# Kernel tuning notes

Hardware: AMD Instinct MI355X
Metric: run time of the kernel (lower is better)

The kernel has to match this reference:

```python
import jax, jax.numpy as jnp
import numpy as np

EPS = 1e-5

def _conv(x, w, pad):
    return jax.lax.conv_general_dilated(
        x, w, window_strides=(1, 1), padding=[(pad, pad), (pad, pad)],
        dimension_numbers=('NCHW', 'OIHW', 'NCHW'))

def _bn(x, g, b):
    # training-mode batch norm over (N, H, W), matching nn.BatchNorm2d in train mode
    m = x.mean(axis=(0, 2, 3), keepdims=True)
    v = x.var(axis=(0, 2, 3), keepdims=True)
    return (x - m) * jax.lax.rsqrt(v + EPS) * g[None, :, None, None] + b[None, :, None, None]

def setup_inputs() -> dict:
    key = jax.random.key(0)
    ks = jax.random.split(key, 16)
    B, C, H, W = 64, 16, 128, 128
    f32 = jnp.float32
    x = jax.random.normal(ks[0], (B, C, H, W), dtype=f32)
    # conv weights (OIHW), He-ish scale
    conv_w1 = jax.random.normal(ks[1], (32, 16, 1, 1), f32) * (2.0 / 16) ** 0.5
    conv_w2 = jax.random.normal(ks[2], (64, 32, 1, 1), f32) * (2.0 / 32) ** 0.5
    conv_w3 = jax.random.normal(ks[3], (32, 64, 3, 3), f32) * (2.0 / (64 * 9)) ** 0.5
    conv_w4 = jax.random.normal(ks[4], (32, 32, 3, 3), f32) * (2.0 / (32 * 9)) ** 0.5
    bn1_g = jnp.ones((32,), f32); bn1_b = jnp.zeros((32,), f32)
    bn2_g = jnp.ones((64,), f32); bn2_b = jnp.zeros((64,), f32)
    bn3_g = jnp.ones((32,), f32); bn3_b = jnp.zeros((32,), f32)
    bn4_g = jnp.ones((32,), f32); bn4_b = jnp.zeros((32,), f32)
    fc1_w = jax.random.normal(ks[5], (32, 32), f32) * (1.0 / 32) ** 0.5
    fc1_b = jnp.zeros((32,), f32)
    fc2_w = jax.random.normal(ks[6], (16, 32), f32) * (1.0 / 32) ** 0.5
    fc2_b = jnp.zeros((16,), f32)
    return dict(x=x, conv_w1=conv_w1, bn1_g=bn1_g, bn1_b=bn1_b,
                conv_w2=conv_w2, bn2_g=bn2_g, bn2_b=bn2_b,
                conv_w3=conv_w3, bn3_g=bn3_g, bn3_b=bn3_b,
                conv_w4=conv_w4, bn4_g=bn4_g, bn4_b=bn4_b,
                fc1_w=fc1_w, fc1_b=fc1_b, fc2_w=fc2_w, fc2_b=fc2_b)

def reference(x, conv_w1, bn1_g, bn1_b, conv_w2, bn2_g, bn2_b,
              conv_w3, bn3_g, bn3_b, conv_w4, bn4_g, bn4_b,
              fc1_w, fc1_b, fc2_w, fc2_b):
    B, C, H, W = x.shape  # C == 16
    # spectral: 1x1 convs
    h = jax.nn.relu(_bn(_conv(x, conv_w1, 0), bn1_g, bn1_b))
    h = jax.nn.relu(_bn(_conv(h, conv_w2, 0), bn2_g, bn2_b))
    # spatial: 3x3 convs
    h = jax.nn.relu(_bn(_conv(h, conv_w3, 1), bn3_g, bn3_b))
    x2 = jax.nn.relu(_bn(_conv(h, conv_w4, 1), bn4_g, bn4_b))  # [B,32,H,W]
    tok = x2.reshape(B, 32, H * W).transpose(0, 2, 1)  # [B,HW,32]
    h1 = jnp.tanh(tok @ fc1_w.T + fc1_b)
    w0 = jnp.tanh(h1 @ fc2_w.T + fc2_b)  # [B,HW,16]
    # y0 is computed BEFORE the torch in-place diag zeroing, which never
    # affects any returned value (w0 is unused afterwards) -> omitted.
    y0 = w0.mean(axis=1)  # [B,16]
    Cm = jnp.einsum('bi,bj->bij', y0, y0)  # [B,16,16]
    wn = jnp.linalg.norm(Cm, axis=2)  # [B,16]
    order = jnp.argsort(-wn, axis=-1)  # descending sort indices
    vals = jnp.take_along_axis(wn, order, axis=-1)  # sorted values
    idx = order[:, :15]  # 5 groups of 3 channels
    gath = jnp.take_along_axis(x, idx[:, :, None, None], axis=1)  # [B,15,H,W]
    fi = gath.reshape(B, 5, 3, H, W).transpose(1, 0, 2, 3, 4)  # [5,B,3,H,W]
    wi = vals[:, :15].reshape(B, 5, 3).mean(axis=-1).T  # [5,B]
    cgh = jnp.einsum('bij,bjn->bin', Cm, x.reshape(B, C, H * W))  # [B,16,HW]
    return (fi, wi, vals, order, cgh)
```

## Files before the change

### kernel.cpp

```cpp
#include <hip/hip_runtime.h>

#define TPB 256

static constexpr int   HWc  = 16384;
static constexpr float NINV = 1.0f / 1048576.0f;

static constexpr unsigned FI_OFF    = 0u;
static constexpr unsigned WI_OFF    = 15728640u;
static constexpr unsigned VALS_OFF  = 15728960u;
static constexpr unsigned ORDER_OFF = 15729984u;
static constexpr unsigned CGH_OFF   = 15731008u;

typedef _Float16 f16;
typedef f16   f16x8 __attribute__((ext_vector_type(8)));
typedef f16   f16x4 __attribute__((ext_vector_type(4)));
typedef float f32x4 __attribute__((ext_vector_type(4)));

__device__ __forceinline__ void gl_lds16(const void* g, void* l) {
    __builtin_amdgcn_global_load_lds(
        (const __attribute__((address_space(1))) unsigned int*)g,
        (__attribute__((address_space(3))) unsigned int*)l, 16, 0, 0);
}

__device__ __forceinline__ float wave_sum(float v) {
#pragma unroll
    for (int o = 1; o < 64; o <<= 1) v += __shfl_xor(v, o, 64);
    return v;
}

__global__ __launch_bounds__(TPB) void k_gramx(const float* __restrict__ x,
                                               float* __restrict__ bkt) {
    __shared__ float red[4][272];
    int tid = threadIdx.x, lane = tid & 63, w = tid >> 6;
    int p = lane & 15, g = lane >> 4;
    const f16 one = (f16)1.0f;
    const f16x8 kOnes = {one, one, one, one, one, one, one, one};
    f32x4 accG = {0.f, 0.f, 0.f, 0.f};
    f32x4 accS = {0.f, 0.f, 0.f, 0.f};
    unsigned wgid = blockIdx.x * 4u + (unsigned)w;
    for (unsigned c = wgid; c < 32768u; c += 2048u) {
        unsigned P0 = c * 32u;
        unsigned b = P0 >> 14, off = P0 & 16383u;
        const float* src = x + ((size_t)b * 16 + p) * HWc + off + g * 8;
        float4 a4 = *(const float4*)src;
        float4 b4 = *(const float4*)(src + 4);
        f16x8 f = { (f16)a4.x, (f16)a4.y, (f16)a4.z, (f16)a4.w,
                    (f16)b4.x, (f16)b4.y, (f16)b4.z, (f16)b4.w };
        accG = __builtin_amdgcn_mfma_f32_16x16x32_f16(f, f, accG, 0, 0, 0);
        accS = __builtin_amdgcn_mfma_f32_16x16x32_f16(kOnes, f, accS, 0, 0, 0);
    }
#pragma unroll
    for (int r = 0; r < 4; ++r) red[w][(4 * g + r) * 16 + p] = accG[r];
    if (g == 0) red[w][256 + p] = accS[0];
    __syncthreads();
    for (int e = tid; e < 272; e += TPB) {
        float v = red[0][e] + red[1][e] + red[2][e] + red[3][e];
        atomicAdd(&bkt[(blockIdx.x & 63u) * 272u + (unsigned)e], v);
    }
}

__global__ void k_sfin1g(const float* __restrict__ bkt, const float* __restrict__ w1,
                         const float* __restrict__ g1, const float* __restrict__ bb1,
                         float* __restrict__ prm) {
    __shared__ float G[256];
    __shared__ float S[16];
    int tid = threadIdx.x;
    {
        float v = 0.f;
        for (int s = 0; s < 64; ++s) v += bkt[s * 272 + tid];
        G[tid] = v;
    }
    if (tid < 16) {
        float v = 0.f;
        for (int s = 0; s < 64; ++s) v += bkt[s * 272 + 256 + tid];
        S[tid] = v;
    }
    __syncthreads();
    if (tid < 32) {
        float wv[16];
#pragma unroll
        for (int i = 0; i < 16; ++i) wv[i] = w1[tid * 16 + i];
        float m = 0.f, e2 = 0.f;
#pragma unroll
        for (int i = 0; i < 16; ++i) {
            m += wv[i] * S[i];
            float t = 0.f;
#pragma unroll
            for (int j = 0; j < 16; ++j) t += wv[j] * G[i * 16 + j];
            e2 += wv[i] * t;
        }
        float mean = m * NINV;
        float var = e2 * NINV - mean * mean;
        float sc = g1[tid] * rsqrtf(var + 1e-5f);
        prm[tid * 2] = sc;
        prm[tid * 2 + 1] = bb1[tid] - mean * sc;
    }
}

__global__ __launch_bounds__(TPB) void k_conv2m(const float* __restrict__ x,
                                                const float* __restrict__ w1,
                                                const float* __restrict__ w2,
                                                const float* __restrict__ prm1,
                                                f16* __restrict__ t2r,
                                                float* __restrict__ bkt) {
    __shared__ __align__(16) float w1s[512];
    __shared__ float p1[64];
    __shared__ __align__(16) f16 V[256 * 40];
    __shared__ float red[4][800];
    int tid = threadIdx.x, lane = tid & 63, w = tid >> 6;
    int p = lane & 15, g = lane >> 4;
    for (int e = tid; e < 512; e += TPB) w1s[e] = w1[e];
    if (tid < 64) p1[tid] = prm1[tid];
    f16x8 Wf[4];
#pragma unroll
    for (int cb = 0; cb < 4; ++cb) {
        const float* wr = w2 + (cb * 16 + p) * 32 + g * 8;
        float4 a4 = *(const float4*)wr;
        float4 b4 = *(const float4*)(wr + 4);
        Wf[cb] = (f16x8){ (f16)a4.x, (f16)a4.y, (f16)a4.z, (f16)a4.w,
                          (f16)b4.x, (f16)b4.y, (f16)b4.z, (f16)b4.w };
    }
    __syncthreads();
    unsigned pid = blockIdx.x * TPB + tid;
    const float* xp = x + (size_t)(pid >> 14) * 16 * HWc + (pid & 16383u);
    float xv[16];
#pragma unroll
    for (int c = 0; c < 16; ++c) xv[c] = xp[(size_t)c * HWc];
    f16* vp = V + tid * 40;
#pragma unroll
    for (int c8 = 0; c8 < 4; ++c8) {
        f16x8 hv;
#pragma unroll
        for (int j = 0; j < 8; ++j) {
            int co = c8 * 8 + j;
            float a = 0.f;
#pragma unroll
            for (int c4 = 0; c4 < 4; ++c4) {
                float4 ww = *(const float4*)&w1s[co * 16 + c4 * 4];
                a = fmaf(xv[c4 * 4 + 0], ww.x, a); a = fmaf(xv[c4 * 4 + 1], ww.y, a);
                a = fmaf(xv[c4 * 4 + 2], ww.z, a); a = fmaf(xv[c4 * 4 + 3], ww.w, a);
            }
            hv[j] = (f16)fmaxf(0.f, fmaf(a, p1[co * 2], p1[co * 2 + 1]));
        }
        *(f16x8*)(vp + c8 * 8) = hv;
    }
    __syncthreads();
    unsigned Pb = blockIdx.x * TPB + (unsigned)(w * 64);
#pragma unroll
    for (int f = 0; f < 4; ++f) {
        int pxl = w * 64 + f * 16 + p;
        f16x8 bf = *(const f16x8*)&V[pxl * 40 + g * 8];
        unsigned Pg = Pb + (unsigned)(f * 16 + p);
#pragma unroll
        for (int cb = 0; cb < 4; ++cb) {
            f32x4 d = {0.f, 0.f, 0.f, 0.f};
            d = __builtin_amdgcn_mfma_f32_16x16x32_f16(Wf[cb], bf, d, 0, 0, 0);
            f16x4 o4 = { (f16)d[0], (f16)d[1], (f16)d[2], (f16)d[3] };
            *(f16x4*)(t2r + (size_t)Pg * 64 + cb * 16 + 4 * g) = o4;
        }
    }
    const f16 one = (f16)1.0f;
    const f16x8 kOnes = {one, one, one, one, one, one, one, one};
    f32x4 accG[3] = {{0.f,0.f,0.f,0.f},{0.f,0.f,0.f,0.f},{0.f,0.f,0.f,0.f}};
    f32x4 accS[2] = {{0.f,0.f,0.f,0.f},{0.f,0.f,0.f,0.f}};
#pragma unroll
    for (int c2 = 0; c2 < 2; ++c2) {
        int px0 = w * 64 + c2 * 32;
        f16x8 fb[2];
#pragma unroll
        for (int cb2 = 0; cb2 < 2; ++cb2)
#pragma unroll
            for (int j = 0; j < 8; ++j)
                fb[cb2][j] = V[(px0 + g * 8 + j) * 40 + cb2 * 16 + p];
        accG[0] = __builtin_amdgcn_mfma_f32_16x16x32_f16(fb[0], fb[0], accG[0], 0, 0, 0);
        accG[1] = __builtin_amdgcn_mfma_f32_16x16x32_f16(fb[0], fb[1], accG[1], 0, 0, 0);
        accG[2] = __builtin_amdgcn_mfma_f32_16x16x32_f16(fb[1], fb[1], accG[2], 0, 0, 0);
        accS[0] = __builtin_amdgcn_mfma_f32_16x16x32_f16(kOnes, fb[0], accS[0], 0, 0, 0);
        accS[1] = __builtin_amdgcn_mfma_f32_16x16x32_f16(kOnes, fb[1], accS[1], 0, 0, 0);
    }
#pragma unroll
    for (int blk = 0; blk < 3; ++blk)
#pragma unroll
        for (int r = 0; r < 4; ++r)
            red[w][blk * 256 + (4 * g + r) * 16 + p] = accG[blk][r];
    if (g == 0) { red[w][768 + p] = accS[0][0]; red[w][784 + p] = accS[1][0]; }
    __syncthreads();
    for (int e = tid; e < 800; e += TPB) {
        float v = red[0][e] + red[1][e] + red[2][e] + red[3][e];
        atomicAdd(&bkt[(blockIdx.x & 63u) * 800u + (unsigned)e], v);
    }
}

__global__ void k_sfin2g(const float* __restrict__ bkt, const float* __restrict__ w2,
                         const float* __restrict__ g2, const float* __restrict__ bb2,
                         float* __restrict__ prm) {
    __shared__ float G[768];
    __shared__ float S[32];
    int tid = threadIdx.x;
    for (int e = tid; e < 768; e += 256) {
        float v = 0.f;
        for (int s = 0; s < 64; ++s) v += bkt[s * 800 + e];
        G[e] = v;
    }
    if (tid < 32) {
        float v = 0.f;
        for (int s = 0; s < 64; ++s) v += bkt[s * 800 + 768 + tid];
        S[tid] = v;
    }
    __syncthreads();
    if (tid < 64) {
        float wv[32];
#pragma unroll
        for (int i = 0; i < 32; ++i) wv[i] = (float)(f16)w2[tid * 32 + i];
        float m = 0.f, e2 = 0.f;
#pragma unroll
        for (int i = 0; i < 32; ++i) {
            m += wv[i] * S[i];
            int bi = i >> 4, il = i & 15;
            float t = 0.f;
#pragma unroll
            for (int j = 0; j < 32; ++j) {
                int bj = j >> 4, jl = j & 15;
                float Gij;
                if (bi <= bj) Gij = G[(bi == 0 ? (bj == 0 ? 0 : 1) : 2) * 256 + il * 16 + jl];
                else          Gij = G[(bj == 0 ? 1 : 2) * 256 + jl * 16 + il];
                t += wv[j] * Gij;
            }
            e2 += wv[i] * t;
        }
        float mean = m * NINV;
        float var = e2 * NINV - mean * mean;
        float sc = g2[tid] * rsqrtf(var + 1e-5f);
        prm[tid * 2] = sc;
        prm[tid * 2 + 1] = bb2[tid] - mean * sc;
    }
}

__global__ void k_sfin(const float* __restrict__ bkt, const float* __restrict__ g,
                       const float* __restrict__ bb, float* __restrict__ prm, int C) {
    int co = threadIdx.x;
    float s = 0.f, q = 0.f;
    for (int k = 0; k < 64; ++k) { s += bkt[(k * C + co) * 2]; q += bkt[(k * C + co) * 2 + 1]; }
    float mean = s * NINV;
    float var = q * NINV - mean * mean;
    float sc = g[co] * rsqrtf(var + 1e-5f);
    prm[co * 2] = sc;
    prm[co * 2 + 1] = bb[co] - mean * sc;
}

template <int CI>
__global__ void k_wprep(const float* __restrict__ w, float* __restrict__ wsg) {
    constexpr int KS = CI / 32;
    int t = blockIdx.x * 256 + threadIdx.x;
    if (t >= KS * 18 * 64) return;
    int lane = t & 63, fr = t >> 6;
    int cf = fr & 1, tap = (fr >> 1) % 9, ks = fr / 18;
    int g = lane >> 4, p = lane & 15;
    int co = cf * 16 + p;
    f16x8 hv;
#pragma unroll
    for (int j = 0; j < 8; ++j) {
        int ci = ks * 32 + g * 8 + j;
        hv[j] = (f16)w[(co * CI + ci) * 9 + tap];
    }
    ((f16x8*)wsg)[fr * 64 + lane] = hv;
}

template <int CI>
__global__ __launch_bounds__(512, 4) void k_conv3(const f16* __restrict__ in,
                                                  const float* __restrict__ wsg,
                                                  const float* __restrict__ prm,
                                                  f16* __restrict__ outp,
                                                  float* __restrict__ bkt) {
    constexpr int KS = CI / 32;
    __shared__ __align__(16) struct {
        f16   Wl[18 * 512];
        f16   Al[6 * 128 * 32];
        float red[8][64];
    } sh;
    int tid = threadIdx.x;
    int lane = tid & 63, w = tid >> 6;
    int p = lane & 15, g = lane >> 4;
    int rw = w >> 1, h = w & 1;
    int cw = tid & 3, pxt = tid >> 2;

    unsigned o = blockIdx.x;
    unsigned xcd = o & 7u, q = o >> 3;
    unsigned rg = q & 31u, grp = q >> 5;
    unsigned b = (grp << 3) | xcd;
    int y0 = (int)rg * 4;

    float psc[KS][8], psh[KS][8];
#pragma unroll
    for (int ks = 0; ks < KS; ++ks)
#pragma unroll
        for (int j = 0; j < 8; ++j) {
            int ch = ks * 32 + cw * 8 + j;
            psc[ks][j] = prm[ch * 2];
            psh[ks][j] = prm[ch * 2 + 1];
        }

    bool mask0 = (h == 0 && p == 0);
    bool mask1 = (h == 1 && p == 15);
    const f16x8 kZ = {0, 0, 0, 0, 0, 0, 0, 0};

    f32x4 acc[4][2];
#pragma unroll
    for (int f = 0; f < 4; ++f)
#pragma unroll
        for (int cf = 0; cf < 2; ++cf) acc[f][cf] = (f32x4){0.f, 0.f, 0.f, 0.f};

    for (int ks = 0; ks < KS; ++ks) {
        if (ks) __syncthreads();
#pragma unroll
        for (int c0 = 0; c0 < 1152; c0 += 512) {
            if (c0 + (w << 6) < 1152) {
                int c = c0 + tid;
                gl_lds16(wsg + (size_t)(ks * 4608 + c * 4), &sh.Wl[c * 8]);
            }
        }
#pragma unroll
        for (int r6 = 0; r6 < 6; ++r6) {
            int yy = y0 - 1 + r6;
            f16* dst = &sh.Al[r6 * 4096 + tid * 8];
            if ((unsigned)yy < 128u) {
                const f16* s = in + ((size_t)(b * 128u + (unsigned)yy) * 128u + pxt) * CI
                                  + ks * 32 + cw * 8;
                f16x8 raw = *(const f16x8*)s;
                f16x8 o8;
#pragma unroll
                for (int j = 0; j < 8; ++j)
                    o8[j] = (f16)fmaxf(0.f, fmaf((float)raw[j], psc[ks][j], psh[ks][j]));
                *(f16x8*)dst = o8;
            } else {
                *(f16x8*)dst = kZ;
            }
        }
        __syncthreads();
        const f16x8* Wv = (const f16x8*)sh.Wl;
        for (int dyi = 0; dyi < 3; ++dyi) {
            int ar = rw + dyi;
#pragma unroll
            for (int dxi = 0; dxi < 3; ++dxi) {
                int tap = dyi * 3 + dxi;
                f16x8 b0 = Wv[(tap * 2 + 0) * 64 + lane];
                f16x8 b1 = Wv[(tap * 2 + 1) * 64 + lane];
#pragma unroll
                for (int f = 0; f < 4; ++f) {
                    int px = h * 64 + f * 16 + p + dxi - 1;
                    f16x8 a = *(const f16x8*)&sh.Al[(ar * 128 + px) * 32 + g * 8];
                    if (dxi == 0 && f == 0) { if (mask0) a = kZ; }
                    if (dxi == 2 && f == 3) { if (mask1) a = kZ; }
                    acc[f][0] = __builtin_amdgcn_mfma_f32_16x16x32_f16(b0, a, acc[f][0], 0, 0, 0);
                    acc[f][1] = __builtin_amdgcn_mfma_f32_16x16x32_f16(b1, a, acc[f][1], 0, 0, 0);
                }
            }
        }
    }

    float sv[8], qv[8];
#pragma unroll
    for (int cf = 0; cf < 2; ++cf)
#pragma unroll
        for (int r = 0; r < 4; ++r) {
            float s = acc[0][cf][r] + acc[1][cf][r] + acc[2][cf][r] + acc[3][cf][r];
            float qq = acc[0][cf][r] * acc[0][cf][r] + acc[1][cf][r] * acc[1][cf][r] +
                       acc[2][cf][r] * acc[2][cf][r] + acc[3][cf][r] * acc[3][cf][r];
#pragma unroll
            for (int m = 1; m < 16; m <<= 1) {
                s += __shfl_xor(s, m, 64);
                qq += __shfl_xor(qq, m, 64);
            }
            sv[cf * 4 + r] = s; qv[cf * 4 + r] = qq;
        }
    if (p == 0) {
#pragma unroll
        for (int cf = 0; cf < 2; ++cf)
#pragma unroll
            for (int r = 0; r < 4; ++r) {
                int co = cf * 16 + g * 4 + r;
                sh.red[w][co * 2] = sv[cf * 4 + r];
                sh.red[w][co * 2 + 1] = qv[cf * 4 + r];
            }
    }

    unsigned pxb = b * 16384u + (unsigned)((y0 + rw) * 128 + h * 64 + p);
#pragma unroll
    for (int f = 0; f < 4; ++f)
#pragma unroll
        for (int cf = 0; cf < 2; ++cf) {
            f16x4 o4 = { (f16)acc[f][cf][0], (f16)acc[f][cf][1],
                         (f16)acc[f][cf][2], (f16)acc[f][cf][3] };
            *(f16x4*)(outp + (size_t)(pxb + f * 16u) * 32u + (unsigned)(cf * 16 + g * 4)) = o4;
        }

    __syncthreads();
    if (tid < 64) {
        float v = 0.f;
#pragma unroll
        for (int ww = 0; ww < 8; ++ww) v += sh.red[ww][tid];
        atomicAdd(&bkt[(o & 63u) * 64u + (unsigned)tid], v);
    }
}

__global__ __launch_bounds__(TPB) void k_fc(const f16* __restrict__ t4,
                                            const float* __restrict__ prm4,
                                            const float* __restrict__ fw1,
                                            const float* __restrict__ fb1,
                                            const float* __restrict__ fw2,
                                            const float* __restrict__ fb2,
                                            float* __restrict__ y0sum) {
    __shared__ __align__(16) float w1s[1024];
    __shared__ __align__(16) float w2s[512];
    __shared__ float b1s[32], b2s[16], p4[64];
    __shared__ float red[4][16];
    int tid = threadIdx.x;
    for (int e = tid; e < 1024; e += TPB) w1s[e] = fw1[e];
    for (int e = tid; e < 512; e += TPB) w2s[e] = fw2[e];
    if (tid < 32) b1s[tid] = fb1[tid];
    if (tid < 16) b2s[tid] = fb2[tid];
    if (tid < 64) p4[tid] = prm4[tid];
    __syncthreads();
    unsigned pid = blockIdx.x * TPB + tid;
    const f16x8* tv = (const f16x8*)(t4 + (size_t)pid * 32);
    float v[32];
#pragma unroll
    for (int c8 = 0; c8 < 4; ++c8) {
        f16x8 raw = tv[c8];
#pragma unroll
        for (int j = 0; j < 8; ++j) {
            int c = c8 * 8 + j;
            v[c] = fmaxf(0.f, fmaf((float)raw[j], p4[c * 2], p4[c * 2 + 1]));
        }
    }
    float hh[32];
#pragma unroll
    for (int j = 0; j < 32; ++j) {
        float a = b1s[j];
#pragma unroll
        for (int c8 = 0; c8 < 8; ++c8) {
            float4 w = *(const float4*)&w1s[j * 32 + c8 * 4];
            a = fmaf(v[c8 * 4 + 0], w.x, a); a = fmaf(v[c8 * 4 + 1], w.y, a);
            a = fmaf(v[c8 * 4 + 2], w.z, a); a = fmaf(v[c8 * 4 + 3], w.w, a);
        }
        hh[j] = tanhf(a);
    }
    unsigned bb = pid >> 14;
    int wv = tid >> 6;
    for (int k = 0; k < 16; ++k) {
        float a = b2s[k];
#pragma unroll
        for (int c8 = 0; c8 < 8; ++c8) {
            float4 w = *(const float4*)&w2s[k * 32 + c8 * 4];
            a = fmaf(hh[c8 * 4 + 0], w.x, a); a = fmaf(hh[c8 * 4 + 1], w.y, a);
            a = fmaf(hh[c8 * 4 + 2], w.z, a); a = fmaf(hh[c8 * 4 + 3], w.w, a);
        }
        a = tanhf(a);
        float s = wave_sum(a);
        if ((tid & 63) == 0) red[wv][k] = s;
    }
    __syncthreads();
    if (tid < 16) {
        float s = red[0][tid] + red[1][tid] + red[2][tid] + red[3][tid];
        atomicAdd(&y0sum[bb * 16u + tid], s);
    }
}

__global__ void k_final(const float* __restrict__ y0sum, float* __restrict__ out,
                        float* __restrict__ Cm, int* __restrict__ idxb) {
    int b = threadIdx.x;
    float y0[16]; float nrm = 0.f;
#pragma unroll
    for (int i = 0; i < 16; ++i) { y0[i] = y0sum[b * 16 + i] * (1.0f / 16384.0f); nrm += y0[i] * y0[i]; }
    nrm = sqrtf(nrm);
    float wn[16]; int id[16];
#pragma unroll
    for (int i = 0; i < 16; ++i) { wn[i] = fabsf(y0[i]) * nrm; id[i] = i; }
    for (int i = 1; i < 16; ++i) {
        float k = wn[i]; int ii = id[i]; int j = i - 1;
        while (j >= 0 && wn[j] < k) { wn[j + 1] = wn[j]; id[j + 1] = id[j]; --j; }
        wn[j + 1] = k; id[j + 1] = ii;
    }
    for (int i = 0; i < 16; ++i) {
        out[VALS_OFF + b * 16 + i] = wn[i];
        out[ORDER_OFF + b * 16 + i] = (float)id[i];
    }
    for (int g = 0; g < 5; ++g)
        out[WI_OFF + g * 64 + b] = (wn[g * 3] + wn[g * 3 + 1] + wn[g * 3 + 2]) * (1.0f / 3.0f);
    for (int i = 0; i < 16; ++i)
        for (int j = 0; j < 16; ++j) Cm[b * 256 + i * 16 + j] = y0[i] * y0[j];
    for (int s = 0; s < 15; ++s) idxb[b * 15 + s] = id[s];
}

__global__ __launch_bounds__(TPB) void k_out(const float* __restrict__ x,
                                             const float* __restrict__ Cm,
                                             const int* __restrict__ idxb,
                                             float* __restrict__ out) {
    __shared__ float cm[256];
    __shared__ int idl[15];
    int tid = threadIdx.x;
    unsigned b = blockIdx.x >> 6;
    unsigned p = ((blockIdx.x & 63u) << 8) + tid;
    cm[tid] = Cm[b * 256u + tid];
    if (tid < 15) idl[tid] = idxb[b * 15u + tid];
    __syncthreads();
    const float* xp = x + (size_t)b * 16 * HWc + p;
    float xv[16];
#pragma unroll
    for (int j = 0; j < 16; ++j) xv[j] = xp[(size_t)j * HWc];
    float* og = out + CGH_OFF + (size_t)b * 16 * HWc + p;
    for (int i = 0; i < 16; ++i) {
        float a = 0.f;
#pragma unroll
        for (int j = 0; j < 16; ++j) a = fmaf(cm[i * 16 + j], xv[j], a);
        og[(size_t)i * HWc] = a;
    }
#pragma unroll
    for (int s = 0; s < 15; ++s) {
        int ch = idl[s];
        float vv = xp[(size_t)ch * HWc];
        int g = s / 3, r = s - 3 * g;
        out[(size_t)((g * 64 + (int)b) * 3 + r) * HWc + p] = vv;
    }
}

extern "C" void kernel_launch(void* const* d_in, const int* in_sizes, int n_in,
                              void* d_out, int out_size, void* d_ws, size_t ws_size,
                              hipStream_t stream) {
    const float* x    = (const float*)d_in[0];
    const float* w1   = (const float*)d_in[1];
    const float* bn1g = (const float*)d_in[2];  const float* bn1b = (const float*)d_in[3];
    const float* w2   = (const float*)d_in[4];
    const float* bn2g = (const float*)d_in[5];  const float* bn2b = (const float*)d_in[6];
    const float* w3   = (const float*)d_in[7];
    const float* bn3g = (const float*)d_in[8];  const float* bn3b = (const float*)d_in[9];
    const float* w4   = (const float*)d_in[10];
    const float* bn4g = (const float*)d_in[11]; const float* bn4b = (const float*)d_in[12];
    const float* fw1  = (const float*)d_in[13]; const float* fb1  = (const float*)d_in[14];
    const float* fw2  = (const float*)d_in[15]; const float* fb2  = (const float*)d_in[16];
    float* out = (float*)d_out;
    float* wsf = (float*)d_ws;

    f16*   t2r = (f16*)wsf;
    f16*   t3r = (f16*)(wsf + 33554432);
    f16*   t4h = (f16*)(wsf + 50331648);
    float* acc = wsf + 67108864;
    float* b1g = acc;
    float* b2g = acc + 17408;
    float* b3  = acc + 68608;
    float* b4  = acc + 76800;
    float* y0s = acc + 84992;
    float* pr1 = acc + 86016;  float* pr2 = acc + 86080;
    float* pr3 = acc + 86208;  float* pr4 = acc + 86272;
    float* Cm  = acc + 86336;
    int*   idxb = (int*)(acc + 102720);
    float* wsg3 = acc + 103680;
    float* wsg4 = acc + 112896;
    size_t need = (size_t)(67108864 + 117504) * 4;
    if (ws_size < need) return;

    hipMemsetAsync(acc, 0, 86016 * 4, stream);

    k_wprep<64><<<9, 256, 0, stream>>>(w3, wsg3);
    k_wprep<32><<<5, 256, 0, stream>>>(w4, wsg4);
    k_gramx<<<512, TPB, 0, stream>>>(x, b1g);
    k_sfin1g<<<1, 256, 0, stream>>>(b1g, w1, bn1g, bn1b, pr1);
    k_conv2m<<<4096, TPB, 0, stream>>>(x, w1, w2, pr1, t2r, b2g);
    k_sfin2g<<<1, 256, 0, stream>>>(b2g, w2, bn2g, bn2b, pr2);
    k_conv3<64><<<2048, 512, 0, stream>>>(t2r, wsg3, pr2, t3r, b3);
    k_sfin<<<1, 32, 0, stream>>>(b3, bn3g, bn3b, pr3, 32);
    k_conv3<32><<<2048, 512, 0, stream>>>(t3r, wsg4, pr3, t4h, b4);
    k_sfin<<<1, 32, 0, stream>>>(b4, bn4g, bn4b, pr4, 32);
    k_fc<<<4096, TPB, 0, stream>>>(t4h, pr4, fw1, fb1, fw2, fb2, y0s);
    k_final<<<1, 64, 0, stream>>>(y0s, out, Cm, idxb);
    k_out<<<4096, TPB, 0, stream>>>(x, Cm, idxb, out);
}
```

Before: 421.5 us.

## Run FC head on MFMA with split-f16 weights and fast tanh

Replaces the per-thread scalar FP32 FC1/FC2 matmuls with 16x16x32 f16 MFMA instructions. Activations are staged through LDS in f16, and weights are split into high and low f16 parts to keep near-FP32 weight precision. The tanhf calls are swapped for an exp-based fast tanh, and the per-batch reduction now uses partial shuffles. This cuts the VALU-bound FMA and transcendental cost, at the price of f16 rounding on activations and hidden values.

```diff
diff --git a/kernel.cpp b/kernel.cpp
--- a/kernel.cpp
+++ b/kernel.cpp
@@ -26,6 +26,11 @@
 #pragma unroll
     for (int o = 1; o < 64; o <<= 1) v += __shfl_xor(v, o, 64);
     return v;
+}
+
+__device__ __forceinline__ float tanh_fast(float x) {
+    float e = __expf(x + x);
+    return 1.0f - __fdividef(2.0f, e + 1.0f);
 }
 
 __global__ __launch_bounds__(TPB) void k_gramx(const float* __restrict__ x,
@@ -403,66 +408,110 @@
     }
 }
 
-__global__ __launch_bounds__(TPB) void k_fc(const f16* __restrict__ t4,
-                                            const float* __restrict__ prm4,
-                                            const float* __restrict__ fw1,
-                                            const float* __restrict__ fb1,
-                                            const float* __restrict__ fw2,
-                                            const float* __restrict__ fb2,
-                                            float* __restrict__ y0sum) {
-    __shared__ __align__(16) float w1s[1024];
-    __shared__ __align__(16) float w2s[512];
-    __shared__ float b1s[32], b2s[16], p4[64];
-    __shared__ float red[4][16];
-    int tid = threadIdx.x;
-    for (int e = tid; e < 1024; e += TPB) w1s[e] = fw1[e];
-    for (int e = tid; e < 512; e += TPB) w2s[e] = fw2[e];
-    if (tid < 32) b1s[tid] = fb1[tid];
-    if (tid < 16) b2s[tid] = fb2[tid];
-    if (tid < 64) p4[tid] = prm4[tid];
+__global__ __launch_bounds__(TPB) void k_fcm(const f16* __restrict__ t4,
+                                             const float* __restrict__ prm4,
+                                             const float* __restrict__ fw1,
+                                             const float* __restrict__ fb1,
+                                             const float* __restrict__ fw2,
+                                             const float* __restrict__ fb2,
+                                             float* __restrict__ y0sum) {
+    __shared__ __align__(16) struct {
+        f16   V1[256 * 40];
+        f16   V2[256 * 40];
+        float p4[64], b1s[32], b2s[16];
+        float red[4][16];
+    } sh;
+    int tid = threadIdx.x, lane = tid & 63, w = tid >> 6;
+    int p = lane & 15, g = lane >> 4;
+    if (tid < 64) sh.p4[tid] = prm4[tid];
+    if (tid < 32) sh.b1s[tid] = fb1[tid];
+    if (tid < 16) sh.b2s[tid] = fb2[tid];
+    f16x8 W1h[2], W1l[2], W2h, W2l;
+#pragma unroll
+    for (int cb = 0; cb < 2; ++cb) {
+        const float* wr = fw1 + (cb * 16 + p) * 32 + g * 8;
+#pragma unroll
+        for (int j = 0; j < 8; ++j) {
+            float v = wr[j];
+            f16 hh = (f16)v;
+            W1h[cb][j] = hh;
+            W1l[cb][j] = (f16)(v - (float)hh);
+        }
+    }
+    {
+        const float* wr = fw2 + p * 32 + g * 8;
+#pragma unroll
+        for (int j = 0; j < 8; ++j) {
+            float v = wr[j];
+            f16 hh = (f16)v;
+            W2h[j] = hh;
+            W2l[j] = (f16)(v - (float)hh);
+        }
+    }
     __syncthreads();
     unsigned pid = blockIdx.x * TPB + tid;
     const f16x8* tv = (const f16x8*)(t4 + (size_t)pid * 32);
-    float v[32];
+    f16* vp = sh.V1 + tid * 40;
 #pragma unroll
     for (int c8 = 0; c8 < 4; ++c8) {
         f16x8 raw = tv[c8];
+        f16x8 o8;
 #pragma unroll
         for (int j = 0; j < 8; ++j) {
             int c = c8 * 8 + j;
-            v[c] = fmaxf(0.f, fmaf((float)raw[j], p4[c * 2], p4[c * 2 + 1]));
-        }
-    }
-    float hh[32];
-#pragma unroll
-    for (int j = 0; j < 32; ++j) {
-        float a = b1s[j];
-#pragma unroll
-        for (int c8 = 0; c8 < 8; ++c8) {
-            float4 w = *(const float4*)&w1s[j * 32 + c8 * 4];
-            a = fmaf(v[c8 * 4 + 0], w.x, a); a = fmaf(v[c8 * 4 + 1], w.y, a);
-            a = fmaf(v[c8 * 4 + 2], w.z, a); a = fmaf(v[c8 * 4 + 3], w.w, a);
-        }
-        hh[j] = tanhf(a);
-    }
-    unsigned bb = pid >> 14;
-    int wv = tid >> 6;
-    for (int k = 0; k < 16; ++k) {
-        float a = b2s[k];
-#pragma unroll
-        for (int c8 = 0; c8 < 8; ++c8) {
-            float4 w = *(const float4*)&w2s[k * 32 + c8 * 4];
-            a = fmaf(hh[c8 * 4 + 0], w.x, a); a = fmaf(hh[c8 * 4 + 1], w.y, a);
-            a = fmaf(hh[c8 * 4 + 2], w.z, a); a = fmaf(hh[c8 * 4 + 3], w.w, a);
-        }
-        a = tanhf(a);
-        float s = wave_sum(a);
-        if ((tid & 63) == 0) red[wv][k] = s;
+            o8[j] = (f16)fmaxf(0.f, fmaf((float)raw[j], sh.p4[c * 2], sh.p4[c * 2 + 1]));
+        }
+        *(f16x8*)(vp + c8 * 8) = o8;
+    }
+    __syncthreads();
+    float bb1[8];
+#pragma unroll
+    for (int cb = 0; cb < 2; ++cb)
+#pragma unroll
+        for (int r = 0; r < 4; ++r) bb1[cb * 4 + r] = sh.b1s[cb * 16 + g * 4 + r];
+#pragma unroll
+    for (int f = 0; f < 4; ++f) {
+        int pxl = w * 64 + f * 16 + p;
+        f16x8 bf = *(const f16x8*)&sh.V1[pxl * 40 + g * 8];
+#pragma unroll
+        for (int cb = 0; cb < 2; ++cb) {
+            f32x4 d = {0.f, 0.f, 0.f, 0.f};
+            d = __builtin_amdgcn_mfma_f32_16x16x32_f16(W1l[cb], bf, d, 0, 0, 0);
+            d = __builtin_amdgcn_mfma_f32_16x16x32_f16(W1h[cb], bf, d, 0, 0, 0);
+            f16x4 h4;
+#pragma unroll
+            for (int r = 0; r < 4; ++r) h4[r] = (f16)tanh_fast(d[r] + bb1[cb * 4 + r]);
+            *(f16x4*)&sh.V2[pxl * 40 + cb * 16 + g * 4] = h4;
+        }
+    }
+    __syncthreads();
+    float bb2[4];
+#pragma unroll
+    for (int r = 0; r < 4; ++r) bb2[r] = sh.b2s[g * 4 + r];
+    float s4[4] = {0.f, 0.f, 0.f, 0.f};
+#pragma unroll
+    for (int f = 0; f < 4; ++f) {
+        int pxl = w * 64 + f * 16 + p;
+        f16x8 bf = *(const f16x8*)&sh.V2[pxl * 40 + g * 8];
+        f32x4 d = {0.f, 0.f, 0.f, 0.f};
+        d = __builtin_amdgcn_mfma_f32_16x16x32_f16(W2l, bf, d, 0, 0, 0);
+        d = __builtin_amdgcn_mfma_f32_16x16x32_f16(W2h, bf, d, 0, 0, 0);
+#pragma unroll
+        for (int r = 0; r < 4; ++r) s4[r] += tanh_fast(d[r] + bb2[r]);
+    }
+#pragma unroll
+    for (int r = 0; r < 4; ++r) {
+#pragma unroll
+        for (int m = 1; m < 16; m <<= 1) s4[r] += __shfl_xor(s4[r], m, 64);
+    }
+    if (p == 0) {
+#pragma unroll
+        for (int r = 0; r < 4; ++r) sh.red[w][g * 4 + r] = s4[r];
     }
     __syncthreads();
     if (tid < 16) {
-        float s = red[0][tid] + red[1][tid] + red[2][tid] + red[3][tid];
-        atomicAdd(&y0sum[bb * 16u + tid], s);
+        float s = sh.red[0][tid] + sh.red[1][tid] + sh.red[2][tid] + sh.red[3][tid];
+        atomicAdd(&y0sum[(blockIdx.x >> 6) * 16u + tid], s);
     }
 }
 
@@ -571,7 +620,7 @@
     k_sfin<<<1, 32, 0, stream>>>(b3, bn3g, bn3b, pr3, 32);
     k_conv3<32><<<2048, 512, 0, stream>>>(t3r, wsg4, pr3, t4h, b4);
     k_sfin<<<1, 32, 0, stream>>>(b4, bn4g, bn4b, pr4, 32);
-    k_fc<<<4096, TPB, 0, stream>>>(t4h, pr4, fw1, fb1, fw2, fb2, y0s);
+    k_fcm<<<4096, TPB, 0, stream>>>(t4h, pr4, fw1, fb1, fw2, fb2, y0s);
     k_final<<<1, 64, 0, stream>>>(y0s, out, Cm, idxb);
     k_out<<<4096, TPB, 0, stream>>>(x, Cm, idxb, out);
 }
```

Result: faster. 365.6 us (-13.3%).
